# Kernel optimization log

Measured on AMD Instinct MI355X. Metric: run time of the kernel, lower is better.

The kernel has to match this reference:

```python
import jax, jax.numpy as jnp
import numpy as np

K = 512  # number of largest entries to KEEP per row (module's k)


def _topk_keep(x, k):
    """Zero all but the k largest entries along the last axis.

    Matches torch: topk(-x, dim-k) finds the (dim-k) smallest values of x
    and scatters 0 into them, keeping the k largest. We implement the
    equivalent keep-mask via top_k indices of x itself (ties resolved by
    index order, same as torch.topk).
    """
    shp = x.shape
    d = shp[-1]
    x2 = x.reshape(-1, d)                      # [N, d]
    _, idx = jax.lax.top_k(x2, k)              # [N, k] indices of largest
    rows = jnp.arange(x2.shape[0])[:, None]    # [N, 1]
    mask = jnp.zeros_like(x2).at[rows, idx].set(1.0)
    return (x2 * mask).reshape(shp)


def setup_inputs() -> dict:
    key = jax.random.key(0)
    x = jax.random.normal(key, (4, 4096, 4096), dtype=jnp.float32)
    return {"x": x}


def reference(x):
    return _topk_keep(x, K)
```

## Files before the change

### kernel.cpp

```cpp
#include <hip/hip_runtime.h>

#define D     4096
#define KKEEP 512
#define TPB   256
#define NSEG  4
#define NB    2048
#define BPT   (NB / TPB)
#define HA(d) ((d) + ((d) >> 3))
#define HWORDS (NB + NB / 8)

__device__ __forceinline__ unsigned key_of(float f) {
    unsigned u = __float_as_uint(f);
    return (u & 0x80000000u) ? ~u : (u | 0x80000000u);
}
__device__ __forceinline__ float val_of(unsigned k) {
    unsigned u = (k & 0x80000000u) ? (k ^ 0x80000000u) : ~k;
    return __uint_as_float(u);
}

__global__ __launch_bounds__(TPB, 8)
void topk_keep_kernel(const float* __restrict__ x, float* __restrict__ out) {
    const int tid = threadIdx.x;
    const unsigned lane = tid & 63u, wid = (unsigned)tid >> 6;
    const float4* px = (const float4*)(x + (long)blockIdx.x * D);
    float4*       po = (float4*)(out + (long)blockIdx.x * D);

    unsigned k[NSEG * 4];
    {
        float4 f0 = px[tid], f1 = px[tid + TPB], f2 = px[tid + 2 * TPB], f3 = px[tid + 3 * TPB];
        k[ 0]=key_of(f0.x); k[ 1]=key_of(f0.y); k[ 2]=key_of(f0.z); k[ 3]=key_of(f0.w);
        k[ 4]=key_of(f1.x); k[ 5]=key_of(f1.y); k[ 6]=key_of(f1.z); k[ 7]=key_of(f1.w);
        k[ 8]=key_of(f2.x); k[ 9]=key_of(f2.y); k[10]=key_of(f2.z); k[11]=key_of(f2.w);
        k[12]=key_of(f3.x); k[13]=key_of(f3.y); k[14]=key_of(f3.z); k[15]=key_of(f3.w);
    }

    __shared__ unsigned hist[HWORDS];
    __shared__ unsigned s_wtot[4];
    __shared__ unsigned s_sel[2];
    __shared__ unsigned s_w01[4];
    __shared__ unsigned s_w23[4];

    unsigned prefix = 0;
    unsigned rem = KKEEP;

    #pragma unroll
    for (int r = 0; r < 3; ++r) {
        const int shift = (r == 0) ? 21 : (r == 1) ? 10 : 0;
        const unsigned mask = (r == 2) ? 1023u : 2047u;

        #pragma unroll
        for (int i = 0; i < 9; ++i) hist[tid + i * TPB] = 0;
        __syncthreads();

        if (r == 0) {
            #pragma unroll
            for (int j = 0; j < 16; ++j)
                atomicAdd(&hist[HA(k[j] >> 21)], 1u);
        } else {
            const int hs = (r == 1) ? 21 : 10;
            #pragma unroll
            for (int j = 0; j < 16; ++j)
                if ((k[j] >> hs) == (prefix >> hs))
                    atomicAdd(&hist[HA((k[j] >> shift) & mask)], 1u);
        }
        __syncthreads();

        unsigned c[BPT];
        unsigned ct = 0;
        {
            const int hb = tid * 9;
            #pragma unroll
            for (int i = 0; i < BPT; ++i) { c[i] = hist[hb + i]; ct += c[i]; }
        }
        unsigned s = ct;
        #pragma unroll
        for (int off = 1; off < 64; off <<= 1) {
            unsigned t = __shfl_down(s, off, 64);
            if (lane + (unsigned)off < 64u) s += t;
        }
        if (lane == 0) s_wtot[wid] = s;
        __syncthreads();
        unsigned above = s - ct;
        #pragma unroll
        for (unsigned w = 0; w < 4; ++w)
            if (w > wid) above += s_wtot[w];
        unsigned run = above;
        #pragma unroll
        for (int i = BPT - 1; i >= 0; --i) {
            unsigned incl = run + c[i];
            if (incl >= rem && run < rem) {
                s_sel[0] = (unsigned)(tid * BPT + i);
                s_sel[1] = rem - run;
            }
            run = incl;
        }
        __syncthreads();
        prefix |= s_sel[0] << shift;
        rem = s_sel[1];
    }

    const unsigned tkey = prefix;

    unsigned e[NSEG];
    #pragma unroll
    for (int j = 0; j < NSEG; ++j) {
        unsigned c0 = (k[4*j+0] == tkey), c1 = (k[4*j+1] == tkey);
        unsigned c2 = (k[4*j+2] == tkey), c3 = (k[4*j+3] == tkey);
        e[j] = c0 + c1 + c2 + c3;
    }
    unsigned p01 = e[0] | (e[1] << 16);
    unsigned p23 = e[2] | (e[3] << 16);
    unsigned i01 = p01, i23 = p23;
    #pragma unroll
    for (int off = 1; off < 64; off <<= 1) {
        unsigned t0 = __shfl_up(i01, off, 64);
        unsigned t1 = __shfl_up(i23, off, 64);
        if (lane >= (unsigned)off) { i01 += t0; i23 += t1; }
    }
    if (lane == 63) { s_w01[wid] = i01; s_w23[wid] = i23; }
    __syncthreads();
    unsigned x01 = i01 - p01, x23 = i23 - p23;
    #pragma unroll
    for (unsigned w = 0; w < 4; ++w)
        if (w < wid) { x01 += s_w01[w]; x23 += s_w23[w]; }
    const unsigned tot01 = s_w01[0] + s_w01[1] + s_w01[2] + s_w01[3];
    const unsigned tot23 = s_w23[0] + s_w23[1] + s_w23[2] + s_w23[3];
    const unsigned total0 = tot01 & 0xffffu, total1 = tot01 >> 16;
    const unsigned total2 = tot23 & 0xffffu;
    unsigned rank[NSEG];
    rank[0] = (x01 & 0xffffu);
    rank[1] = total0 + (x01 >> 16);
    rank[2] = total0 + total1 + (x23 & 0xffffu);
    rank[3] = total0 + total1 + total2 + (x23 >> 16);

    #pragma unroll
    for (int j = 0; j < NSEG; ++j) {
        float4 o;
        unsigned eqr = rank[j];
        float* ofp = (float*)&o;
        #pragma unroll
        for (int c = 0; c < 4; ++c) {
            unsigned kk = k[4*j + c];
            bool keep;
            if (kk > tkey)       keep = true;
            else if (kk == tkey) { keep = (eqr < rem); ++eqr; }
            else                 keep = false;
            ofp[c] = keep ? val_of(kk) : 0.0f;
        }
        po[tid + j * TPB] = o;
    }
}

extern "C" void kernel_launch(void* const* d_in, const int* in_sizes, int n_in,
                              void* d_out, int out_size, void* d_ws, size_t ws_size,
                              hipStream_t stream) {
    const float* x = (const float*)d_in[0];
    float* out = (float*)d_out;
    const int rows = in_sizes[0] / D;
    topk_keep_kernel<<<dim3(rows), dim3(TPB), 0, stream>>>(x, out);
}
```

Measured before the change: 431.5 us.

## Use 512-thread blocks with 4-way salted shared histogram to cut atomic contention

```diff
diff --git a/kernel.cpp b/kernel.cpp
--- a/kernel.cpp
+++ b/kernel.cpp
@@ -2,12 +2,13 @@
 
 #define D     4096
 #define KKEEP 512
-#define TPB   256
-#define NSEG  4
+#define TPB   512
+#define NSEG  2
 #define NB    2048
 #define BPT   (NB / TPB)
-#define HA(d) ((d) + ((d) >> 3))
-#define HWORDS (NB + NB / 8)
+#define SALT  4
+#define HWORDS (NB * SALT)
+#define NWAVE (TPB / 64)
 
 __device__ __forceinline__ unsigned key_of(float f) {
     unsigned u = __float_as_uint(f);
@@ -18,27 +19,25 @@
     return __uint_as_float(u);
 }
 
-__global__ __launch_bounds__(TPB, 8)
+__global__ __launch_bounds__(TPB, 4)
 void topk_keep_kernel(const float* __restrict__ x, float* __restrict__ out) {
     const int tid = threadIdx.x;
     const unsigned lane = tid & 63u, wid = (unsigned)tid >> 6;
+    const unsigned salt = lane & (SALT - 1u);
     const float4* px = (const float4*)(x + (long)blockIdx.x * D);
     float4*       po = (float4*)(out + (long)blockIdx.x * D);
 
     unsigned k[NSEG * 4];
     {
-        float4 f0 = px[tid], f1 = px[tid + TPB], f2 = px[tid + 2 * TPB], f3 = px[tid + 3 * TPB];
-        k[ 0]=key_of(f0.x); k[ 1]=key_of(f0.y); k[ 2]=key_of(f0.z); k[ 3]=key_of(f0.w);
-        k[ 4]=key_of(f1.x); k[ 5]=key_of(f1.y); k[ 6]=key_of(f1.z); k[ 7]=key_of(f1.w);
-        k[ 8]=key_of(f2.x); k[ 9]=key_of(f2.y); k[10]=key_of(f2.z); k[11]=key_of(f2.w);
-        k[12]=key_of(f3.x); k[13]=key_of(f3.y); k[14]=key_of(f3.z); k[15]=key_of(f3.w);
+        float4 f0 = px[tid], f1 = px[tid + TPB];
+        k[0]=key_of(f0.x); k[1]=key_of(f0.y); k[2]=key_of(f0.z); k[3]=key_of(f0.w);
+        k[4]=key_of(f1.x); k[5]=key_of(f1.y); k[6]=key_of(f1.z); k[7]=key_of(f1.w);
     }
 
-    __shared__ unsigned hist[HWORDS];
-    __shared__ unsigned s_wtot[4];
+    __shared__ __align__(16) unsigned hist[HWORDS];
+    __shared__ unsigned s_wtot[NWAVE];
     __shared__ unsigned s_sel[2];
-    __shared__ unsigned s_w01[4];
-    __shared__ unsigned s_w23[4];
+    __shared__ unsigned s_p[NWAVE];
 
     unsigned prefix = 0;
     unsigned rem = KKEEP;
@@ -48,29 +47,40 @@
         const int shift = (r == 0) ? 21 : (r == 1) ? 10 : 0;
         const unsigned mask = (r == 2) ? 1023u : 2047u;
 
-        #pragma unroll
-        for (int i = 0; i < 9; ++i) hist[tid + i * TPB] = 0;
+        {
+            uint4 z = make_uint4(0u, 0u, 0u, 0u);
+            uint4* hz = (uint4*)&hist[tid * (BPT * SALT)];
+            hz[0] = z; hz[1] = z; hz[2] = z; hz[3] = z;
+        }
         __syncthreads();
 
         if (r == 0) {
             #pragma unroll
-            for (int j = 0; j < 16; ++j)
-                atomicAdd(&hist[HA(k[j] >> 21)], 1u);
+            for (int j = 0; j < 8; ++j) {
+                unsigned b = k[j] >> 21;
+                atomicAdd(&hist[(b << 2) | salt], 1u);
+            }
         } else {
             const int hs = (r == 1) ? 21 : 10;
             #pragma unroll
-            for (int j = 0; j < 16; ++j)
-                if ((k[j] >> hs) == (prefix >> hs))
-                    atomicAdd(&hist[HA((k[j] >> shift) & mask)], 1u);
+            for (int j = 0; j < 8; ++j)
+                if ((k[j] >> hs) == (prefix >> hs)) {
+                    unsigned b = (k[j] >> shift) & mask;
+                    atomicAdd(&hist[(b << 2) | salt], 1u);
+                }
         }
         __syncthreads();
 
         unsigned c[BPT];
         unsigned ct = 0;
         {
-            const int hb = tid * 9;
+            const uint4* hb = (const uint4*)&hist[tid * (BPT * SALT)];
             #pragma unroll
-            for (int i = 0; i < BPT; ++i) { c[i] = hist[hb + i]; ct += c[i]; }
+            for (int i = 0; i < BPT; ++i) {
+                uint4 w = hb[i];
+                c[i] = w.x + w.y + w.z + w.w;
+                ct += c[i];
+            }
         }
         unsigned s = ct;
         #pragma unroll
@@ -82,7 +92,7 @@
         __syncthreads();
         unsigned above = s - ct;
         #pragma unroll
-        for (unsigned w = 0; w < 4; ++w)
+        for (unsigned w = 0; w < NWAVE; ++w)
             if (w > wid) above += s_wtot[w];
         unsigned run = above;
         #pragma unroll
@@ -101,37 +111,28 @@
 
     const unsigned tkey = prefix;
 
-    unsigned e[NSEG];
-    #pragma unroll
-    for (int j = 0; j < NSEG; ++j) {
-        unsigned c0 = (k[4*j+0] == tkey), c1 = (k[4*j+1] == tkey);
-        unsigned c2 = (k[4*j+2] == tkey), c3 = (k[4*j+3] == tkey);
-        e[j] = c0 + c1 + c2 + c3;
-    }
-    unsigned p01 = e[0] | (e[1] << 16);
-    unsigned p23 = e[2] | (e[3] << 16);
-    unsigned i01 = p01, i23 = p23;
+    unsigned e0 = (k[0]==tkey) + (k[1]==tkey) + (k[2]==tkey) + (k[3]==tkey);
+    unsigned e1 = (k[4]==tkey) + (k[5]==tkey) + (k[6]==tkey) + (k[7]==tkey);
+    unsigned p = e0 | (e1 << 16);
+    unsigned ip = p;
     #pragma unroll
     for (int off = 1; off < 64; off <<= 1) {
-        unsigned t0 = __shfl_up(i01, off, 64);
-        unsigned t1 = __shfl_up(i23, off, 64);
-        if (lane >= (unsigned)off) { i01 += t0; i23 += t1; }
+        unsigned t = __shfl_up(ip, off, 64);
+        if (lane >= (unsigned)off) ip += t;
     }
-    if (lane == 63) { s_w01[wid] = i01; s_w23[wid] = i23; }
+    if (lane == 63) s_p[wid] = ip;
     __syncthreads();
-    unsigned x01 = i01 - p01, x23 = i23 - p23;
+    unsigned xp = ip - p;
     #pragma unroll
-    for (unsigned w = 0; w < 4; ++w)
-        if (w < wid) { x01 += s_w01[w]; x23 += s_w23[w]; }
-    const unsigned tot01 = s_w01[0] + s_w01[1] + s_w01[2] + s_w01[3];
-    const unsigned tot23 = s_w23[0] + s_w23[1] + s_w23[2] + s_w23[3];
-    const unsigned total0 = tot01 & 0xffffu, total1 = tot01 >> 16;
-    const unsigned total2 = tot23 & 0xffffu;
+    for (unsigned w = 0; w < NWAVE; ++w)
+        if (w < wid) xp += s_p[w];
+    unsigned tot = 0;
+    #pragma unroll
+    for (unsigned w = 0; w < NWAVE; ++w) tot += s_p[w];
+    const unsigned total0 = tot & 0xffffu;
     unsigned rank[NSEG];
-    rank[0] = (x01 & 0xffffu);
-    rank[1] = total0 + (x01 >> 16);
-    rank[2] = total0 + total1 + (x23 & 0xffffu);
-    rank[3] = total0 + total1 + total2 + (x23 >> 16);
+    rank[0] = xp & 0xffffu;
+    rank[1] = total0 + (xp >> 16);
 
     #pragma unroll
     for (int j = 0; j < NSEG; ++j) {
@@ -139,13 +140,13 @@
         unsigned eqr = rank[j];
         float* ofp = (float*)&o;
         #pragma unroll
-        for (int c = 0; c < 4; ++c) {
-            unsigned kk = k[4*j + c];
+        for (int c2 = 0; c2 < 4; ++c2) {
+            unsigned kk = k[4*j + c2];
             bool keep;
             if (kk > tkey)       keep = true;
             else if (kk == tkey) { keep = (eqr < rem); ++eqr; }
             else                 keep = false;
-            ofp[c] = keep ? val_of(kk) : 0.0f;
+            ofp[c2] = keep ? val_of(kk) : 0.0f;
         }
         po[tid + j * TPB] = o;
     }
```

After: 534.0 us. 1.24x slower.
